# Optimization experiments

Hardware: AMD Instinct MI355X
Metric: run time of the kernel (lower is better)

## Reference

```python
import jax, jax.numpy as jnp
import numpy as np

B = 8192       # Monte Carlo paths
NSTEP = 30     # Euler time steps
D = 100        # z_dim / number of assets
H1 = 110
H2 = 110
T = NSTEP - 1  # number of subnets
DT = np.float32(1.0 / NSTEP)
R = np.float32(0.05)   # riskfree
EPS = np.float32(1e-3) # Keras BatchNormalization epsilon


def setup_inputs() -> dict:
    key = jax.random.key(0)
    ks = jax.random.split(key, 25)
    f = jnp.float32
    X = jax.random.normal(ks[0], (B, NSTEP, D), f)
    DWs = jax.random.normal(ks[1], (B, NSTEP, D), f) * jnp.sqrt(DT)
    sigmas = jax.random.uniform(ks[2], (D,), f, 0.1, 0.4)
    y_init = jax.random.uniform(ks[3], (1,), f, 0.0, 1.0)
    z_init = jax.random.uniform(ks[4], (1, D), f, -0.1, 0.1)
    W1 = jax.random.normal(ks[5], (T, D, H1), f) / np.sqrt(D).astype(np.float32)
    W2 = jax.random.normal(ks[6], (T, H1, H2), f) / np.sqrt(H1).astype(np.float32)
    W3 = jax.random.normal(ks[7], (T, H2, D), f) / np.sqrt(H2).astype(np.float32)
    dims = [D, H1, H2, D]
    bn = {}
    for j, dim in enumerate(dims):
        bn[f"g{j}"] = 1.0 + 0.1 * jax.random.normal(ks[8 + 4 * j], (T, dim), f)
        bn[f"b{j}"] = 0.05 * jax.random.normal(ks[9 + 4 * j], (T, dim), f)
        bn[f"m{j}"] = 0.1 * jax.random.normal(ks[10 + 4 * j], (T, dim), f)
        bn[f"v{j}"] = jax.random.uniform(ks[11 + 4 * j], (T, dim), f, 0.5, 1.5)
    return dict(X=X, DWs=DWs, sigmas=sigmas, y_init=y_init, z_init=z_init,
                W1=W1, W2=W2, W3=W3, **bn)


def _bn(x, g, b, m, v):
    # Keras BatchNormalization, inference mode
    return (x - m) * jax.lax.rsqrt(v + EPS) * g + b


def _subnet(x, p):
    (w1, w2, w3, g0, b0, m0, v0, g1, b1, m1, v1,
     g2, b2, m2, v2, g3, b3, m3, v3) = p
    x = _bn(x, g0, b0, m0, v0)
    x = jax.nn.relu(x @ w1)
    x = _bn(x, g1, b1, m1, v1)
    x = jax.nn.relu(x @ w2)
    x = _bn(x, g2, b2, m2, v2)
    x = x @ w3
    return _bn(x, g3, b3, m3, v3)


def reference(X, DWs, sigmas, y_init, z_init, W1, W2, W3,
              g0, b0, m0, v0, g1, b1, m1, v1,
              g2, b2, m2, v2, g3, b3, m3, v3):
    nb = X.shape[0]
    Y0 = jnp.ones((nb, 1), X.dtype) * y_init            # [B,1]
    Z0 = jnp.ones((nb, 1), X.dtype) * z_init            # [B,D]

    def step(carry, xs):
        Y, Z = carry
        Xi, Xn, DWi, p = xs
        Y = Y + R * Y * DT + jnp.sum(sigmas * Xi * Z * DWi, axis=1, keepdims=True)
        Z = _subnet(Xn, p)
        return (Y, Z), None

    params = (W1, W2, W3, g0, b0, m0, v0, g1, b1, m1, v1,
              g2, b2, m2, v2, g3, b3, m3, v3)  # each leading dim T
    xs = (jnp.moveaxis(X[:, :T], 1, 0),        # [T,B,D]
          jnp.moveaxis(X[:, 1:T + 1], 1, 0),   # [T,B,D]
          jnp.moveaxis(DWs[:, :T], 1, 0),      # [T,B,D]
          params)
    (Y, Z), _ = jax.lax.scan(step, (Y0, Z0), xs)
    # final step: X[:,-2,:] with DWs[:,-1,:]
    Y = Y + R * Y * DT + jnp.sum(sigmas * X[:, -2, :] * Z * DWs[:, -1, :],
                                 axis=1, keepdims=True)
    return Y
```

## Files before the change

kernel.cpp:

```cpp
#include <hip/hip_runtime.h>

typedef unsigned short ushort_t;
typedef __attribute__((ext_vector_type(8))) short s16x8;
typedef __attribute__((ext_vector_type(4))) float f32x4;

#define B_PATHS 8192
#define NSTEP   30
#define DD      100
#define HH      110
#define TT      29
#define ROWSTR  3000
#define LDK     136
#define NROWS   112
#define WMATSZ  (128*LDK)
#define DT_C    (1.0f/30.0f)
#define R_C     0.05f
#define EPS_C   1e-3f

__device__ __forceinline__ ushort_t f2bf(float f) {
  unsigned u = __float_as_uint(f);
  u = u + 0x7FFFu + ((u >> 16) & 1u);
  return (ushort_t)(u >> 16);
}

__global__ void prep_kernel(const float* __restrict__ W1, const float* __restrict__ W2,
                            const float* __restrict__ W3,
                            const float* g0, const float* b0, const float* m0, const float* v0,
                            const float* g1, const float* b1, const float* m1, const float* v1,
                            const float* g2, const float* b2, const float* m2, const float* v2,
                            const float* g3, const float* b3, const float* m3, const float* v3,
                            ushort_t* __restrict__ wprep, float* __restrict__ bprep)
{
  const int mat = blockIdx.x, t = blockIdx.y, tid = threadIdx.x;
  __shared__ float wsh[110*110];
  __shared__ float sin_[112], hin_[112], sout_[112], hout_[112];

  int Kr, Nr; const float* W; const float *g, *bb, *mm, *vv;
  if (mat == 0)      { Kr = 100; Nr = 110; W = W1 + t*11000; g = g0+t*100; bb = b0+t*100; mm = m0+t*100; vv = v0+t*100; }
  else if (mat == 1) { Kr = 110; Nr = 110; W = W2 + t*12100; g = g1+t*110; bb = b1+t*110; mm = m1+t*110; vv = v1+t*110; }
  else               { Kr = 110; Nr = 100; W = W3 + t*11000; g = g2+t*110; bb = b2+t*110; mm = m2+t*110; vv = v2+t*110; }

  if (tid < Kr) {
    float s = g[tid] * rsqrtf(vv[tid] + EPS_C);
    sin_[tid] = s; hin_[tid] = bb[tid] - mm[tid]*s;
  }
  if (mat == 2 && tid < Nr) {
    float s = g3[t*100+tid] * rsqrtf(v3[t*100+tid] + EPS_C);
    sout_[tid] = s; hout_[tid] = b3[t*100+tid] - m3[t*100+tid]*s;
  }
  for (int i = tid; i < Kr*Nr; i += 256) wsh[i] = W[i];
  __syncthreads();

  if (tid < 128) {
    float c = 0.f;
    if (tid < Nr) {
      for (int k = 0; k < Kr; ++k) c += hin_[k] * wsh[k*Nr + tid];
      if (mat == 2) c = c * sout_[tid] + hout_[tid];
    }
    bprep[(t*3 + mat)*128 + tid] = c;
  }
  ushort_t* wo = wprep + (size_t)(t*3 + mat) * WMATSZ;
  for (int idx = tid; idx < 128*LDK; idx += 256) {
    int n = idx / LDK, k = idx - n*LDK;
    float v = 0.f;
    if (n < Nr && k < Kr) {
      v = sin_[k] * wsh[k*Nr + n];
      if (mat == 2) v *= sout_[n];
    }
    wo[idx] = f2bf(v);
  }
}

__device__ __forceinline__ void gemm_relu_stage(const ushort_t* actIn, const ushort_t* wb,
                                                const float* __restrict__ biasg,
                                                ushort_t* actOut, int wr, int lrow, int quad)
{
  f32x4 acc[7];
  const f32x4 z4 = {0.f, 0.f, 0.f, 0.f};
#pragma unroll
  for (int nt = 0; nt < 7; ++nt) acc[nt] = z4;
#pragma unroll
  for (int kb = 0; kb < 4; ++kb) {
    s16x8 a = *(const s16x8*)(actIn + (wr + lrow)*LDK + kb*32 + quad*8);
#pragma unroll
    for (int nt = 0; nt < 7; ++nt) {
      s16x8 b = *(const s16x8*)(wb + (nt*16 + lrow)*LDK + kb*32 + quad*8);
      acc[nt] = __builtin_amdgcn_mfma_f32_16x16x32_bf16(a, b, acc[nt], 0, 0, 0);
    }
  }
#pragma unroll
  for (int nt = 0; nt < 7; ++nt) {
    const int col = nt*16 + lrow;
    const float bv = biasg[col];
#pragma unroll
    for (int r = 0; r < 4; ++r) {
      float u = acc[nt][r] + bv;
      u = u > 0.f ? u : 0.f;
      actOut[(wr + quad*4 + r)*LDK + col] = f2bf(u);
    }
  }
}

__global__ __launch_bounds__(256, 2)
void subnet_kernel(const float* __restrict__ X, const float* __restrict__ DW,
                   const float* __restrict__ sigmas,
                   const ushort_t* __restrict__ wprep, const float* __restrict__ bprep,
                   float* __restrict__ sbuf)
{
  __shared__ __align__(16) ushort_t actA[64*LDK];
  __shared__ __align__(16) ushort_t actB[64*LDK];
  __shared__ __align__(16) ushort_t wbuf[NROWS*LDK];

  const int tid  = threadIdx.x;
  const int t    = blockIdx.y;
  const int m0   = blockIdx.x * 64;
  const int lane = tid & 63, lrow = lane & 15, quad = lane >> 4;
  const int wr   = (tid >> 6) * 16;

  {
    const uint4 z4 = {0u, 0u, 0u, 0u};
    uint4* pA = (uint4*)actA; uint4* pB = (uint4*)actB;
    for (int i = tid; i < 1088; i += 256) { pA[i] = z4; pB[i] = z4; }
  }
  __syncthreads();

  for (int j = tid; j < 64*25; j += 256) {
    int r = j / 25, c = j - r*25;
    const float4 v = *(const float4*)(X + (size_t)(m0 + r)*ROWSTR + (t+1)*DD + c*4);
    ushort4 u; u.x = f2bf(v.x); u.y = f2bf(v.y); u.z = f2bf(v.z); u.w = f2bf(v.w);
    *(ushort4*)(actA + r*LDK + c*4) = u;
  }
  {
    const uint4* ws = (const uint4*)(wprep + (size_t)(t*3 + 0)*WMATSZ);
    uint4* wd = (uint4*)wbuf;
    for (int j = tid; j < (NROWS*LDK)/8; j += 256) wd[j] = ws[j];
  }
  __syncthreads();

  gemm_relu_stage(actA, wbuf, bprep + (t*3 + 0)*128, actB, wr, lrow, quad);
  __syncthreads();
  {
    const uint4* ws = (const uint4*)(wprep + (size_t)(t*3 + 1)*WMATSZ);
    uint4* wd = (uint4*)wbuf;
    for (int j = tid; j < (NROWS*LDK)/8; j += 256) wd[j] = ws[j];
  }
  __syncthreads();

  gemm_relu_stage(actB, wbuf, bprep + (t*3 + 1)*128, actA, wr, lrow, quad);
  __syncthreads();
  {
    const uint4* ws = (const uint4*)(wprep + (size_t)(t*3 + 2)*WMATSZ);
    uint4* wd = (uint4*)wbuf;
    for (int j = tid; j < (NROWS*LDK)/8; j += 256) wd[j] = ws[j];
  }
  __syncthreads();

  {
    f32x4 acc[7];
    const f32x4 z4 = {0.f, 0.f, 0.f, 0.f};
#pragma unroll
    for (int nt = 0; nt < 7; ++nt) acc[nt] = z4;
#pragma unroll
    for (int kb = 0; kb < 4; ++kb) {
      s16x8 a = *(const s16x8*)(actA + (wr + lrow)*LDK + kb*32 + quad*8);
#pragma unroll
      for (int nt = 0; nt < 7; ++nt) {
        s16x8 b = *(const s16x8*)(wbuf + (nt*16 + lrow)*LDK + kb*32 + quad*8);
        acc[nt] = __builtin_amdgcn_mfma_f32_16x16x32_bf16(a, b, acc[nt], 0, 0, 0);
      }
    }
    const float* biasg = bprep + (t*3 + 2)*128;
    const int xt = (t == TT - 1) ? (NSTEP - 2) : (t + 1);
    float p[4] = {0.f, 0.f, 0.f, 0.f};
#pragma unroll
    for (int nt = 0; nt < 7; ++nt) {
      const int d = nt*16 + lrow;
      if (d < DD) {
        const float sg = sigmas[d];
        const float bv = biasg[d];
#pragma unroll
        for (int r = 0; r < 4; ++r) {
          const int b = m0 + wr + quad*4 + r;
          const float xv = X[(size_t)b*ROWSTR + xt*DD + d];
          const float dv = DW[(size_t)b*ROWSTR + (t+1)*DD + d];
          const float zv = acc[nt][r] + bv;
          p[r] = fmaf(sg*xv*dv, zv, p[r]);
        }
      }
    }
#pragma unroll
    for (int off = 1; off < 16; off <<= 1) {
#pragma unroll
      for (int r = 0; r < 4; ++r) p[r] += __shfl_xor(p[r], off, 64);
    }
    if (lrow == 0) {
      float4 o; o.x = p[0]; o.y = p[1]; o.z = p[2]; o.w = p[3];
      *(float4*)(sbuf + (size_t)(t+1)*B_PATHS + m0 + wr + quad*4) = o;
    }
  }
}

__global__ void y_kernel(const float* __restrict__ X, const float* __restrict__ DW,
                         const float* __restrict__ sigmas, const float* __restrict__ y_init,
                         const float* __restrict__ z_init, const float* __restrict__ sbuf,
                         float* __restrict__ out)
{
  const int b = blockIdx.x * blockDim.x + threadIdx.x;
  const float* xr = X + (size_t)b * ROWSTR;
  const float* dr = DW + (size_t)b * ROWSTR;
  float s0 = 0.f;
#pragma unroll 5
  for (int c = 0; c < 25; ++c) {
    float4 xv = *(const float4*)(xr + c*4);
    float4 dv = *(const float4*)(dr + c*4);
    float4 sg = *(const float4*)(sigmas + c*4);
    float4 zv = *(const float4*)(z_init + c*4);
    s0 += sg.x*xv.x*zv.x*dv.x;
    s0 += sg.y*xv.y*zv.y*dv.y;
    s0 += sg.z*xv.z*zv.z*dv.z;
    s0 += sg.w*xv.w*zv.w*dv.w;
  }
  float y = y_init[0];
  y = y + R_C*y*DT_C + s0;
  for (int tau = 1; tau < NSTEP; ++tau)
    y = y + R_C*y*DT_C + sbuf[(size_t)tau*B_PATHS + b];
  out[b] = y;
}

extern "C" void kernel_launch(void* const* d_in, const int* in_sizes, int n_in,
                              void* d_out, int out_size, void* d_ws, size_t ws_size,
                              hipStream_t stream) {
  const float* X      = (const float*)d_in[0];
  const float* DWs    = (const float*)d_in[1];
  const float* sigmas = (const float*)d_in[2];
  const float* y_init = (const float*)d_in[3];
  const float* z_init = (const float*)d_in[4];
  const float* W1     = (const float*)d_in[5];
  const float* W2     = (const float*)d_in[6];
  const float* W3     = (const float*)d_in[7];
  const float* bn[16];
  for (int i = 0; i < 16; ++i) bn[i] = (const float*)d_in[8 + i];

  char* ws = (char*)d_ws;
  ushort_t* wprep = (ushort_t*)ws;
  float*    bprep = (float*)(ws + 3028992);
  float*    sbuf  = (float*)(ws + 3073536);
  float*    out   = (float*)d_out;

  prep_kernel<<<dim3(3, TT), 256, 0, stream>>>(
      W1, W2, W3,
      bn[0], bn[1], bn[2], bn[3],  bn[4], bn[5], bn[6], bn[7],
      bn[8], bn[9], bn[10], bn[11], bn[12], bn[13], bn[14], bn[15],
      wprep, bprep);
  subnet_kernel<<<dim3(B_PATHS/64, TT), 256, 0, stream>>>(
      X, DWs, sigmas, wprep, bprep, sbuf);
  y_kernel<<<dim3(B_PATHS/256), 256, 0, stream>>>(
      X, DWs, sigmas, y_init, z_init, sbuf, out);
}
```

Measured before the change: 361.9 us.

## Pre-swizzle weights into MFMA fragment order and read them directly from global

The prep kernel now writes the bf16 weights in per-lane MFMA fragment order, so the subnet kernel loads B fragments straight from global/L2 instead of staging each weight matrix in shared memory with extra barriers. Freeing the weight LDS buffer allows launch bounds to rise to 4 blocks per CU. The final layer now writes its output to LDS as bf16, and a separate coalesced pass computes the sigma*X*DW*Z dot product per row, replacing scattered global reads in the MFMA epilogue. The trade-off is more global traffic for weights and bf16 rounding of Z before the reduction.

Measured after the change: 335.8 us. 7.2% less time.

```diff
diff --git a/kernel.cpp b/kernel.cpp
--- a/kernel.cpp
+++ b/kernel.cpp
@@ -11,8 +11,7 @@
 #define TT      29
 #define ROWSTR  3000
 #define LDK     136
-#define NROWS   112
-#define WMATSZ  (128*LDK)
+#define WFRAGSZ 14336
 #define DT_C    (1.0f/30.0f)
 #define R_C     0.05f
 #define EPS_C   1e-3f
@@ -21,6 +20,9 @@
   unsigned u = __float_as_uint(f);
   u = u + 0x7FFFu + ((u >> 16) & 1u);
   return (ushort_t)(u >> 16);
+}
+__device__ __forceinline__ float bf2f(ushort_t u) {
+  return __uint_as_float(((unsigned)u) << 16);
 }
 
 __global__ void prep_kernel(const float* __restrict__ W1, const float* __restrict__ W2,
@@ -59,33 +61,49 @@
     }
     bprep[(t*3 + mat)*128 + tid] = c;
   }
-  ushort_t* wo = wprep + (size_t)(t*3 + mat) * WMATSZ;
-  for (int idx = tid; idx < 128*LDK; idx += 256) {
-    int n = idx / LDK, k = idx - n*LDK;
-    float v = 0.f;
-    if (n < Nr && k < Kr) {
-      v = sin_[k] * wsh[k*Nr + n];
-      if (mat == 2) v *= sout_[n];
-    }
-    wo[idx] = f2bf(v);
-  }
-}
-
-__device__ __forceinline__ void gemm_relu_stage(const ushort_t* actIn, const ushort_t* wb,
-                                                const float* __restrict__ biasg,
-                                                ushort_t* actOut, int wr, int lrow, int quad)
+
+  ushort_t* wo = wprep + (size_t)(t*3 + mat) * WFRAGSZ;
+  for (int ch = tid; ch < 1792; ch += 256) {
+    const int lane = ch & 63, ntkb = ch >> 6;
+    const int nt = ntkb % 7, kb = ntkb / 7;
+    const int n  = nt*16 + (lane & 15);
+    const int k0 = kb*32 + (lane >> 4)*8;
+    ushort_t tmp[8];
+#pragma unroll
+    for (int j = 0; j < 8; ++j) {
+      const int k = k0 + j;
+      float v = 0.f;
+      if (n < Nr && k < Kr) {
+        v = sin_[k] * wsh[k*Nr + n];
+        if (mat == 2) v *= sout_[n];
+      }
+      tmp[j] = f2bf(v);
+    }
+    ushort4 lo; lo.x = tmp[0]; lo.y = tmp[1]; lo.z = tmp[2]; lo.w = tmp[3];
+    ushort4 hi; hi.x = tmp[4]; hi.y = tmp[5]; hi.z = tmp[6]; hi.w = tmp[7];
+    *(ushort4*)(wo + ch*8)     = lo;
+    *(ushort4*)(wo + ch*8 + 4) = hi;
+  }
+}
+
+__device__ __forceinline__ void mlp_stage(const ushort_t* actIn, const ushort_t* __restrict__ wfrag,
+                                          const float* __restrict__ biasg, ushort_t* actOut,
+                                          int wr, int lane, int lrow, int quad, bool relu)
 {
   f32x4 acc[7];
   const f32x4 z4 = {0.f, 0.f, 0.f, 0.f};
 #pragma unroll
   for (int nt = 0; nt < 7; ++nt) acc[nt] = z4;
+  s16x8 a[4];
+#pragma unroll
+  for (int kb = 0; kb < 4; ++kb)
+    a[kb] = *(const s16x8*)(actIn + (wr + lrow)*LDK + kb*32 + quad*8);
 #pragma unroll
   for (int kb = 0; kb < 4; ++kb) {
-    s16x8 a = *(const s16x8*)(actIn + (wr + lrow)*LDK + kb*32 + quad*8);
 #pragma unroll
     for (int nt = 0; nt < 7; ++nt) {
-      s16x8 b = *(const s16x8*)(wb + (nt*16 + lrow)*LDK + kb*32 + quad*8);
-      acc[nt] = __builtin_amdgcn_mfma_f32_16x16x32_bf16(a, b, acc[nt], 0, 0, 0);
+      s16x8 b = *(const s16x8*)(wfrag + ((kb*7 + nt)*64 + lane)*8);
+      acc[nt] = __builtin_amdgcn_mfma_f32_16x16x32_bf16(a[kb], b, acc[nt], 0, 0, 0);
     }
   }
 #pragma unroll
@@ -95,13 +113,16 @@
 #pragma unroll
     for (int r = 0; r < 4; ++r) {
       float u = acc[nt][r] + bv;
-      u = u > 0.f ? u : 0.f;
+      if (relu) u = u > 0.f ? u : 0.f;
       actOut[(wr + quad*4 + r)*LDK + col] = f2bf(u);
     }
   }
-}
-
-__global__ __launch_bounds__(256, 2)
+#pragma unroll
+  for (int r = 0; r < 4; ++r)
+    actOut[(wr + quad*4 + r)*LDK + 112 + lrow] = 0;
+}
+
+__global__ __launch_bounds__(256, 4)
 void subnet_kernel(const float* __restrict__ X, const float* __restrict__ DW,
                    const float* __restrict__ sigmas,
                    const ushort_t* __restrict__ wprep, const float* __restrict__ bprep,
@@ -109,7 +130,6 @@
 {
   __shared__ __align__(16) ushort_t actA[64*LDK];
   __shared__ __align__(16) ushort_t actB[64*LDK];
-  __shared__ __align__(16) ushort_t wbuf[NROWS*LDK];
 
   const int tid  = threadIdx.x;
   const int t    = blockIdx.y;
@@ -117,86 +137,49 @@
   const int lane = tid & 63, lrow = lane & 15, quad = lane >> 4;
   const int wr   = (tid >> 6) * 16;
 
+  for (int j = tid; j < 64*32; j += 256) {
+    const int r = j >> 5, c = j & 31;
+    ushort4 u; u.x = 0; u.y = 0; u.z = 0; u.w = 0;
+    if (c < 25) {
+      const float4 v = *(const float4*)(X + (size_t)(m0 + r)*ROWSTR + (t+1)*DD + c*4);
+      u.x = f2bf(v.x); u.y = f2bf(v.y); u.z = f2bf(v.z); u.w = f2bf(v.w);
+    }
+    *(ushort4*)(actA + r*LDK + c*4) = u;
+  }
+  __syncthreads();
+
+  const ushort_t* wf = wprep + (size_t)(t*3) * WFRAGSZ;
+  const float*    bg = bprep + (t*3) * 128;
+
+  mlp_stage(actA, wf,             bg,       actB, wr, lane, lrow, quad, true);
+  __syncthreads();
+  mlp_stage(actB, wf + WFRAGSZ,   bg + 128, actA, wr, lane, lrow, quad, true);
+  __syncthreads();
+  mlp_stage(actA, wf + 2*WFRAGSZ, bg + 256, actB, wr, lane, lrow, quad, false);
+  __syncthreads();
+
   {
-    const uint4 z4 = {0u, 0u, 0u, 0u};
-    uint4* pA = (uint4*)actA; uint4* pB = (uint4*)actB;
-    for (int i = tid; i < 1088; i += 256) { pA[i] = z4; pB[i] = z4; }
-  }
-  __syncthreads();
-
-  for (int j = tid; j < 64*25; j += 256) {
-    int r = j / 25, c = j - r*25;
-    const float4 v = *(const float4*)(X + (size_t)(m0 + r)*ROWSTR + (t+1)*DD + c*4);
-    ushort4 u; u.x = f2bf(v.x); u.y = f2bf(v.y); u.z = f2bf(v.z); u.w = f2bf(v.w);
-    *(ushort4*)(actA + r*LDK + c*4) = u;
-  }
-  {
-    const uint4* ws = (const uint4*)(wprep + (size_t)(t*3 + 0)*WMATSZ);
-    uint4* wd = (uint4*)wbuf;
-    for (int j = tid; j < (NROWS*LDK)/8; j += 256) wd[j] = ws[j];
-  }
-  __syncthreads();
-
-  gemm_relu_stage(actA, wbuf, bprep + (t*3 + 0)*128, actB, wr, lrow, quad);
-  __syncthreads();
-  {
-    const uint4* ws = (const uint4*)(wprep + (size_t)(t*3 + 1)*WMATSZ);
-    uint4* wd = (uint4*)wbuf;
-    for (int j = tid; j < (NROWS*LDK)/8; j += 256) wd[j] = ws[j];
-  }
-  __syncthreads();
-
-  gemm_relu_stage(actB, wbuf, bprep + (t*3 + 1)*128, actA, wr, lrow, quad);
-  __syncthreads();
-  {
-    const uint4* ws = (const uint4*)(wprep + (size_t)(t*3 + 2)*WMATSZ);
-    uint4* wd = (uint4*)wbuf;
-    for (int j = tid; j < (NROWS*LDK)/8; j += 256) wd[j] = ws[j];
-  }
-  __syncthreads();
-
-  {
-    f32x4 acc[7];
-    const f32x4 z4 = {0.f, 0.f, 0.f, 0.f};
-#pragma unroll
-    for (int nt = 0; nt < 7; ++nt) acc[nt] = z4;
-#pragma unroll
-    for (int kb = 0; kb < 4; ++kb) {
-      s16x8 a = *(const s16x8*)(actA + (wr + lrow)*LDK + kb*32 + quad*8);
-#pragma unroll
-      for (int nt = 0; nt < 7; ++nt) {
-        s16x8 b = *(const s16x8*)(wbuf + (nt*16 + lrow)*LDK + kb*32 + quad*8);
-        acc[nt] = __builtin_amdgcn_mfma_f32_16x16x32_bf16(a, b, acc[nt], 0, 0, 0);
-      }
-    }
-    const float* biasg = bprep + (t*3 + 2)*128;
-    const int xt = (t == TT - 1) ? (NSTEP - 2) : (t + 1);
-    float p[4] = {0.f, 0.f, 0.f, 0.f};
-#pragma unroll
-    for (int nt = 0; nt < 7; ++nt) {
-      const int d = nt*16 + lrow;
-      if (d < DD) {
-        const float sg = sigmas[d];
-        const float bv = biasg[d];
-#pragma unroll
-        for (int r = 0; r < 4; ++r) {
-          const int b = m0 + wr + quad*4 + r;
-          const float xv = X[(size_t)b*ROWSTR + xt*DD + d];
-          const float dv = DW[(size_t)b*ROWSTR + (t+1)*DD + d];
-          const float zv = acc[nt][r] + bv;
-          p[r] = fmaf(sg*xv*dv, zv, p[r]);
-        }
-      }
-    }
-#pragma unroll
-    for (int off = 1; off < 16; off <<= 1) {
-#pragma unroll
-      for (int r = 0; r < 4; ++r) p[r] += __shfl_xor(p[r], off, 64);
-    }
-    if (lrow == 0) {
-      float4 o; o.x = p[0]; o.y = p[1]; o.z = p[2]; o.w = p[3];
-      *(float4*)(sbuf + (size_t)(t+1)*B_PATHS + m0 + wr + quad*4) = o;
-    }
+    const int row = tid >> 2, part = tid & 3;
+    const int b   = m0 + row;
+    const int xt  = (t == TT - 1) ? (NSTEP - 2) : (t + 1);
+    const float* xr = X  + (size_t)b*ROWSTR + xt*DD;
+    const float* dr = DW + (size_t)b*ROWSTR + (t+1)*DD;
+    float p = 0.f;
+#pragma unroll
+    for (int g = part; g < 25; g += 4) {
+      const float4 xv = *(const float4*)(xr + g*4);
+      const float4 dv = *(const float4*)(dr + g*4);
+      const float4 sg = *(const float4*)(sigmas + g*4);
+      const ushort4 zu = *(const ushort4*)(actB + row*LDK + g*4);
+      p += sg.x*xv.x*dv.x*bf2f(zu.x);
+      p += sg.y*xv.y*dv.y*bf2f(zu.y);
+      p += sg.z*xv.z*dv.z*bf2f(zu.z);
+      p += sg.w*xv.w*dv.w*bf2f(zu.w);
+    }
+    p += __shfl_xor(p, 1, 64);
+    p += __shfl_xor(p, 2, 64);
+    if (part == 0)
+      sbuf[(size_t)(t+1)*B_PATHS + b] = p;
   }
 }
 
@@ -222,6 +205,7 @@
   }
   float y = y_init[0];
   y = y + R_C*y*DT_C + s0;
+#pragma unroll
   for (int tau = 1; tau < NSTEP; ++tau)
     y = y + R_C*y*DT_C + sbuf[(size_t)tau*B_PATHS + b];
   out[b] = y;
@@ -243,8 +227,8 @@
 
   char* ws = (char*)d_ws;
   ushort_t* wprep = (ushort_t*)ws;
-  float*    bprep = (float*)(ws + 3028992);
-  float*    sbuf  = (float*)(ws + 3073536);
+  float*    bprep = (float*)(ws + 2494464);
+  float*    sbuf  = (float*)(ws + 2539008);
   float*    out   = (float*)d_out;
 
   prep_kernel<<<dim3(3, TT), 256, 0, stream>>>(
```
